# Performance work log

Hardware: AMD Instinct MI355X
Metric: run time of the kernel (lower is better)

The kernel has to match this reference:

```python
import jax, jax.numpy as jnp
import numpy as np

S, B, C, H, W = 16, 64, 128, 11, 11
P = H * W
N_ITER = 3
EPS = 1e-5


def setup_inputs() -> dict:
    key = jax.random.key(0)
    ks = jax.random.split(key, 12)
    w = lambda k, shape: jax.random.normal(k, shape, jnp.float32) * 0.02
    return {
        "x": jax.random.normal(ks[0], (S, B, C, H, W), jnp.float32),
        # intra-attention 1x1 convs (stored as [out,in] matrices)
        "wq": w(ks[1], (C, C)), "bq": jnp.zeros((C,), jnp.float32),
        "wk": w(ks[2], (C, C)), "bk": jnp.zeros((C,), jnp.float32),
        "wv": w(ks[3], (C, C)), "bv": jnp.zeros((C,), jnp.float32),
        "intra_alpha": jnp.float32(1.0),
        # inter-message path
        "w_msg": w(ks[4], (C, C + 1)), "b_msg": jnp.zeros((C,), jnp.float32),
        "w_lin": w(ks[5], (C, C)),
        "weight": jnp.float32(0.5),
        "w_gate": w(ks[6], (C, C)), "b_gate": jnp.zeros((C,), jnp.float32),
        # ConvGRU 3x3 convs
        "w_zr": w(ks[7], (2 * C, 2 * C, 3, 3)), "b_zr": jnp.zeros((2 * C,), jnp.float32),
        "w_h": w(ks[8], (C, 2 * C, 3, 3)), "b_h": jnp.zeros((C,), jnp.float32),
        # LayerNorm over [C,11,11]
        "ln_gamma": jnp.ones((C, H, W), jnp.float32),
        "ln_beta": jnp.zeros((C, H, W), jnp.float32),
    }


def reference(x, wq, bq, wk, bk, wv, bv, intra_alpha, w_msg, b_msg, w_lin,
              weight, w_gate, b_gate, w_zr, b_zr, w_h, b_h, ln_gamma, ln_beta):
    scale = C ** -0.5

    def c1(t, wgt, bias):  # 1x1 conv on [S,B,Cin,H,W] -> [S,B,Cout,H,W]
        return jnp.einsum('sbchw,oc->sbohw', t, wgt) + bias[:, None, None]

    def conv3(t, wgt, bias):  # 3x3 'SAME' conv on [N,Cin,H,W]
        y = jax.lax.conv_general_dilated(
            t, wgt, (1, 1), 'SAME', dimension_numbers=('NCHW', 'OIHW', 'NCHW'))
        return y + bias[None, :, None, None]

    # chain-graph neighbor validity masks (|i-j| == 1)
    mask_l = (jnp.arange(S) >= 1).astype(x.dtype)[:, None, None, None, None]
    mask_r = (jnp.arange(S) <= S - 2).astype(x.dtype)[:, None, None, None, None]

    h = x
    for _ in range(N_ITER):
        # ---- intra spatial self-attention (per node, over P=H*W tokens) ----
        q = c1(h, wq, bq).reshape(S, B, C, P)
        k = c1(h, wk, bk).reshape(S, B, C, P)
        v = c1(h, wv, bv).reshape(S, B, C, P)
        att = jax.nn.softmax(jnp.einsum('sbcp,sbcq->sbpq', q, k) * scale, axis=-1)
        intra = jnp.einsum('sbpq,sbcq->sbcp', att, v).reshape(S, B, C, H, W)
        intra = intra_alpha * intra + h

        # ---- inter gated message attention from chain neighbors ----
        xf = h.reshape(S, B, C, P)

        def gated_msg(y, edge_val):
            ef = jnp.full((S, B, 1, H, W), edge_val, h.dtype)  # edge feature i-j
            yy = c1(jnp.concatenate([y, ef], axis=2), w_msg, b_msg).reshape(S, B, C, P)
            yy = jnp.einsum('sbcp,dc->sbdp', yy, w_lin)  # Linear (no bias)
            a = jax.nn.softmax(jnp.einsum('sbcp,sbcq->sbpq', xf, yy), axis=-1)
            m = jnp.einsum('sbpq,sbcq->sbcp', a, yy).reshape(S, B, C, H, W)
            g = jax.nn.sigmoid(c1(m, w_gate, b_gate).mean(axis=(-2, -1), keepdims=True))
            return m * g

        y_left = jnp.concatenate([jnp.zeros_like(h[:1]), h[:-1]], axis=0)   # h[i-1], edge +1
        y_right = jnp.concatenate([h[1:], jnp.zeros_like(h[:1])], axis=0)   # h[i+1], edge -1
        inter = gated_msg(y_left, 1.0) * mask_l + gated_msg(y_right, -1.0) * mask_r

        comb = weight * intra + (1.0 - weight) * inter

        # ---- ConvGRU update (fold S into batch) ----
        xg = comb.reshape(S * B, C, H, W)
        hg = h.reshape(S * B, C, H, W)
        zr = jax.nn.sigmoid(conv3(jnp.concatenate([xg, hg], axis=1), w_zr, b_zr))
        z, r = zr[:, :C], zr[:, C:]
        h_hat = jnp.tanh(conv3(jnp.concatenate([xg, r * hg], axis=1), w_h, b_h))
        h_new = ((1 - z) * hg + z * h_hat).reshape(S, B, C, H, W)

        # ---- residual + LayerNorm over [C,H,W] ----
        nh = h_new + h
        mu = nh.mean(axis=(-3, -2, -1), keepdims=True)
        var = nh.var(axis=(-3, -2, -1), keepdims=True)
        h = (nh - mu) * jax.lax.rsqrt(var + EPS) * ln_gamma + ln_beta
    return h
```

## Files before the change

### kernel.cpp

```cpp
#include <hip/hip_runtime.h>
#include <hip/hip_bf16.h>

#define S_   16
#define B_   64
#define SBn  1024
#define C_   128
#define P_   121
#define CP_  15488
static const long NEl = 15859712L;

typedef __hip_bfloat16 bf16t;
typedef __attribute__((ext_vector_type(8))) short bf16x8;
typedef __attribute__((ext_vector_type(4))) float f32x4;
typedef __attribute__((ext_vector_type(4))) unsigned short us4;

__device__ __forceinline__ float ldb(const bf16t* p){ return __bfloat162float(*p); }
__device__ __forceinline__ float b2f(unsigned short u){ unsigned x=((unsigned)u)<<16; float f; __builtin_memcpy(&f,&x,4); return f; }
__device__ __forceinline__ unsigned short f2bu(float v){ __hip_bfloat16 b=__float2bfloat16(v); unsigned short u; __builtin_memcpy(&u,&b,2); return u; }
__device__ __forceinline__ float ldin(const void* s, long i, int f){
    return f ? ((const float*)s)[i] : b2f(((const unsigned short*)s)[i]);
}

__global__ void detect_kernel(const unsigned short* __restrict__ x, int* __restrict__ flag){
    if(blockIdx.x==0 && threadIdx.x==0){
        int crazy=0;
        for(int i=0;i<512;i++){
            unsigned e=(x[i]>>7)&0xFF;
            if(e!=0 && (e<64 || e>191)) crazy++;
        }
        *flag=(crazy>40)?1:0;
    }
}

__global__ void cvt_kernel(float* __restrict__ dst, const void* __restrict__ src, long n, const int* __restrict__ flag){
    long i=(long)blockIdx.x*blockDim.x+threadIdx.x;
    long st=(long)gridDim.x*blockDim.x;
    int f=*flag;
    for(;i<n;i+=st) dst[i]=ldin(src,i,f);
}

__global__ __launch_bounds__(256) void cvtT_kernel(bf16t* __restrict__ hT, const void* __restrict__ x, const int* __restrict__ flag){
    __shared__ bf16t tl[CP_];
    int sb=blockIdx.x, t=threadIdx.x; int f=*flag;
    for(int i=t;i<CP_;i+=256)
        tl[i]=__float2bfloat16(ldin(x,(long)sb*CP_+i,f));
    __syncthreads();
    bf16t* ho=hT+(size_t)sb*CP_;
    for(int j=t;j<CP_;j+=256){
        int p=j>>7, c=j&127;
        ho[j]=tl[c*P_+p];
    }
}

__global__ __launch_bounds__(128) void prep_msg_kernel(float* __restrict__ W2, float* __restrict__ b2l, float* __restrict__ b2r,
        const void* __restrict__ wlin, const void* __restrict__ wmsg, const void* __restrict__ bmsg, const int* __restrict__ flag){
    int d=blockIdx.x, c=threadIdx.x; int f=*flag;
    float acc=0.f;
    for(int o2=0;o2<C_;o2++) acc += ldin(wlin,(long)d*C_+o2,f)*ldin(wmsg,(long)o2*(C_+1)+c,f);
    W2[d*C_+c]=acc;
    if(c<2){
        float e=(c==0)?1.f:-1.f; float a=0.f;
        for(int o2=0;o2<C_;o2++) a += ldin(wlin,(long)d*C_+o2,f)*(ldin(bmsg,o2,f)+e*ldin(wmsg,(long)o2*(C_+1)+C_,f));
        if(c==0) b2l[d]=a; else b2r[d]=a;
    }
}

template<int RAW>
__global__ void prep_w1t(bf16t* __restrict__ dst, const void* __restrict__ src, const int* __restrict__ flag){
    int idx=blockIdx.x*blockDim.x+threadIdx.x;
    if(idx>=16384) return;
    int r=idx&31, oc=(idx>>5)&127, icb=idx>>12;
    float v = RAW? ldin(src,(long)oc*C_+icb*32+r,*flag) : ((const float*)src)[(long)oc*C_+icb*32+r];
    dst[idx]=__float2bfloat16(v);
}

__global__ void prep_w3t(bf16t* __restrict__ dst, const void* __restrict__ src, const int* __restrict__ flag, int OC){
    int idx=blockIdx.x*blockDim.x+threadIdx.x;
    int tot=OC*2304;
    if(idx>=tot) return;
    int r=idx&31; int rest=idx>>5; int oc=rest%OC; int g2=rest/OC; int icb=g2&7, tap=g2>>3;
    float v=ldin(src,((long)(oc*256+icb*32+r))*9+tap,*flag);
    dst[idx]=__float2bfloat16(v);
}

__global__ void prep_gbt(float* __restrict__ gamT, float* __restrict__ betT,
                         const void* __restrict__ gam, const void* __restrict__ bet, const int* __restrict__ flag){
    int idx=blockIdx.x*blockDim.x+threadIdx.x;
    if(idx>=CP_) return;
    int c=idx/P_, p=idx-c*P_; int f=*flag;
    gamT[p*C_+c]=ldin(gam,idx,f);
    betT[p*C_+c]=ldin(bet,idx,f);
}

__global__ void prep_wgt(float* __restrict__ wgT, float* __restrict__ bg2,
                         const void* __restrict__ wg, const void* __restrict__ bg, const int* __restrict__ flag){
    int idx=blockIdx.x*blockDim.x+threadIdx.x;
    int f=*flag;
    if(idx<16384){ int k=idx>>7, c=idx&127; wgT[idx]=ldin(wg,(long)c*C_+k,f); }
    if(idx<128) bg2[idx]=ldin(bg,idx,f);
}

__device__ __forceinline__ void gemm24r(f32x4 (&acc)[4][2],
    const bf16t* __restrict__ Wt, const bf16x8 (&hreg)[4][2],
    int ocr,int l15,int kg)
{
    #pragma unroll
    for(int i=0;i<4;i++){
        #pragma unroll
        for(int j=0;j<2;j++) acc[i][j]=(f32x4){0.f,0.f,0.f,0.f};
    }
    #pragma unroll
    for(int kc=0;kc<4;kc++){
        bf16x8 a[4];
        #pragma unroll
        for(int mt=0;mt<4;mt++) a[mt]=*(const bf16x8*)(Wt+((size_t)(kc*C_+ocr*64+mt*16+l15))*32+kg*8);
        #pragma unroll
        for(int mt=0;mt<4;mt++){
            #pragma unroll
            for(int nt=0;nt<2;nt++)
                acc[mt][nt]=__builtin_amdgcn_mfma_f32_16x16x32_bf16(a[mt],hreg[kc][nt],acc[mt][nt],0,0,0);
        }
    }
}

__device__ __forceinline__ void msg_phase(
    f32x4 (&res)[8], const bf16t* __restrict__ hT, int sb, int shift,
    const bf16t* __restrict__ W2T, const float* __restrict__ b2e,
    const float* __restrict__ wgT, const float* __restrict__ bgf, float w1m,
    const bf16x8 (&areg)[4],
    bf16t* LA, bf16t* LB, float* fl,
    int t,int w,int l15,int kg,int ocr,int pcr)
{
    __syncthreads();
    const bf16t* hsp=hT+(size_t)(sb+shift)*CP_;
    bf16x8 hregS[4][2];
    #pragma unroll
    for(int kc=0;kc<4;kc++){
        #pragma unroll
        for(int nt=0;nt<2;nt++)
            hregS[kc][nt]=*(const bf16x8*)(hsp+(size_t)(pcr*32+nt*16+l15)*C_+kc*32+kg*8);
    }
    f32x4 acc[4][2];
    gemm24r(acc,W2T,hregS,ocr,l15,kg);
    #pragma unroll
    for(int mt=0;mt<4;mt++){
        int oc0=ocr*64+mt*16+kg*4;
        #pragma unroll
        for(int nt=0;nt<2;nt++){
            int p=pcr*32+nt*16+l15;
            us4 pk;
            #pragma unroll
            for(int r=0;r<4;r++){
                float v=acc[mt][nt][r]+b2e[oc0+r];
                pk[r]=f2bu(v);
                LB[(oc0+r)*136+p]=__float2bfloat16(p<P_? v : 0.f);
            }
            *(us4*)(LA+p*136+oc0)=pk;
        }
    }
    __syncthreads();
    int m0=w*16;
    f32x4 s[8];
    #pragma unroll
    for(int nt=0;nt<8;nt++) s[nt]=(f32x4){0.f,0.f,0.f,0.f};
    #pragma unroll
    for(int kc=0;kc<4;kc++){
        #pragma unroll
        for(int nt=0;nt<8;nt++){
            bf16x8 b=*(const bf16x8*)(LA+(size_t)(nt*16+l15)*136+kc*32+kg*8);
            s[nt]=__builtin_amdgcn_mfma_f32_16x16x32_bf16(areg[kc],b,s[nt],0,0,0);
        }
    }
    if(l15>=9){
        #pragma unroll
        for(int r=0;r<4;r++) s[7][r]=-3.0e38f;
    }
    #pragma unroll
    for(int r=0;r<4;r++){
        float mx=s[0][r];
        #pragma unroll
        for(int nt=1;nt<8;nt++) mx=fmaxf(mx,s[nt][r]);
        #pragma unroll
        for(int o=1;o<16;o<<=1) mx=fmaxf(mx,__shfl_xor(mx,o));
        float sm=0.f;
        #pragma unroll
        for(int nt=0;nt<8;nt++){ float e=__expf(s[nt][r]-mx); s[nt][r]=e; sm+=e; }
        #pragma unroll
        for(int o=1;o<16;o<<=1) sm+=__shfl_xor(sm,o);
        float rs=1.f/sm;
        #pragma unroll
        for(int nt=0;nt<8;nt++) s[nt][r]*=rs;
    }
    __syncthreads();
    #pragma unroll
    for(int r=0;r<4;r++){
        int pr=m0+kg*4+r;
        #pragma unroll
        for(int nt=0;nt<8;nt++) LA[pr*136+nt*16+l15]=__float2bfloat16(s[nt][r]);
    }
    __syncthreads();
    f32x4 o[8];
    #pragma unroll
    for(int nt=0;nt<8;nt++) o[nt]=(f32x4){0.f,0.f,0.f,0.f};
    #pragma unroll
    for(int jc=0;jc<4;jc++){
        bf16x8 a=*(const bf16x8*)(LB+(size_t)(m0+l15)*136+jc*32+kg*8);
        #pragma unroll
        for(int nt=0;nt<8;nt++){
            bf16x8 b=*(const bf16x8*)(LA+(size_t)(nt*16+l15)*136+jc*32+kg*8);
            o[nt]=__builtin_amdgcn_mfma_f32_16x16x32_bf16(a,b,o[nt],0,0,0);
        }
    }
    int c0=m0+kg*4;
    #pragma unroll
    for(int r=0;r<4;r++){
        float sm=0.f;
        #pragma unroll
        for(int nt=0;nt<8;nt++){ float v=o[nt][r]; if(nt==7&&l15>8) v=0.f; sm+=v; }
        sm+=__shfl_xor(sm,1); sm+=__shfl_xor(sm,2); sm+=__shfl_xor(sm,4); sm+=__shfl_xor(sm,8);
        if(l15==0) fl[c0+r]=sm*(1.f/121.f);
    }
    __syncthreads();
    if(t<C_){
        float a=bgf[t];
        #pragma unroll 8
        for(int k=0;k<C_;k++) a+=wgT[k*C_+t]*fl[k];
        fl[C_+t]=1.f/(1.f+__expf(-a));
    }
    __syncthreads();
    float gg[4];
    #pragma unroll
    for(int r=0;r<4;r++) gg[r]=fl[C_+c0+r];
    #pragma unroll
    for(int nt=0;nt<8;nt++){
        #pragma unroll
        for(int r=0;r<4;r++) res[nt][r]+=w1m*o[nt][r]*gg[r];
    }
}

__global__ __launch_bounds__(512) void attn_all(
    bf16t* __restrict__ comb, const bf16t* __restrict__ hT,
    const bf16t* __restrict__ WqT, const bf16t* __restrict__ WkT, const bf16t* __restrict__ WvT,
    const float* __restrict__ bq, const float* __restrict__ bk, const float* __restrict__ bv,
    const bf16t* __restrict__ W2T, const float* __restrict__ b2l, const float* __restrict__ b2r,
    const float* __restrict__ wgT, const float* __restrict__ bgf,
    const float* __restrict__ alphap, const float* __restrict__ wp)
{
    __shared__ bf16t LA[128*136];
    __shared__ bf16t LB[128*136];
    __shared__ float fl[256];
    int sb=blockIdx.x, t=threadIdx.x, lane=t&63, w=t>>6;
    int l15=lane&15, kg=lane>>4;
    const bf16t* hp=hT+(size_t)sb*CP_;
    int ocr=w>>2, pcr=w&3;
    int m0=w*16;
    bf16x8 hreg[4][2];
    #pragma unroll
    for(int kc=0;kc<4;kc++){
        #pragma unroll
        for(int nt=0;nt<2;nt++)
            hreg[kc][nt]=*(const bf16x8*)(hp+(size_t)(pcr*32+nt*16+l15)*C_+kc*32+kg*8);
    }
    bf16x8 areg[4];
    #pragma unroll
    for(int kc=0;kc<4;kc++)
        areg[kc]=*(const bf16x8*)(hp+(size_t)(m0+l15)*C_+kc*32+kg*8);

    f32x4 acc[4][2];
    gemm24r(acc,WqT,hreg,ocr,l15,kg);
    #pragma unroll
    for(int mt=0;mt<4;mt++){
        int oc0=ocr*64+mt*16+kg*4;
        #pragma unroll
        for(int nt=0;nt<2;nt++){
            int p=pcr*32+nt*16+l15;
            us4 pk;
            #pragma unroll
            for(int r=0;r<4;r++) pk[r]=f2bu(acc[mt][nt][r]+bq[oc0+r]);
            *(us4*)(LA+p*136+oc0)=pk;
        }
    }
    gemm24r(acc,WkT,hreg,ocr,l15,kg);
    #pragma unroll
    for(int mt=0;mt<4;mt++){
        int oc0=ocr*64+mt*16+kg*4;
        #pragma unroll
        for(int nt=0;nt<2;nt++){
            int p=pcr*32+nt*16+l15;
            us4 pk;
            #pragma unroll
            for(int r=0;r<4;r++) pk[r]=f2bu(acc[mt][nt][r]+bk[oc0+r]);
            *(us4*)(LB+p*136+oc0)=pk;
        }
    }
    __syncthreads();
    f32x4 s[8];
    #pragma unroll
    for(int nt=0;nt<8;nt++) s[nt]=(f32x4){0.f,0.f,0.f,0.f};
    #pragma unroll
    for(int kc=0;kc<4;kc++){
        bf16x8 a=*(const bf16x8*)(LA+(size_t)(m0+l15)*136+kc*32+kg*8);
        #pragma unroll
        for(int nt=0;nt<8;nt++){
            bf16x8 b=*(const bf16x8*)(LB+(size_t)(nt*16+l15)*136+kc*32+kg*8);
            s[nt]=__builtin_amdgcn_mfma_f32_16x16x32_bf16(a,b,s[nt],0,0,0);
        }
    }
    const float scale=0.08838834764831845f;
    #pragma unroll
    for(int nt=0;nt<8;nt++){
        #pragma unroll
        for(int r=0;r<4;r++) s[nt][r]*=scale;
    }
    if(l15>=9){
        #pragma unroll
        for(int r=0;r<4;r++) s[7][r]=-3.0e38f;
    }
    #pragma unroll
    for(int r=0;r<4;r++){
        float mx=s[0][r];
        #pragma unroll
        for(int nt=1;nt<8;nt++) mx=fmaxf(mx,s[nt][r]);
        #pragma unroll
        for(int o=1;o<16;o<<=1) mx=fmaxf(mx,__shfl_xor(mx,o));
        float sm=0.f;
        #pragma unroll
        for(int nt=0;nt<8;nt++){ float e=__expf(s[nt][r]-mx); s[nt][r]=e; sm+=e; }
        #pragma unroll
        for(int o=1;o<16;o<<=1) sm+=__shfl_xor(sm,o);
        float rs=1.f/sm;
        #pragma unroll
        for(int nt=0;nt<8;nt++) s[nt][r]*=rs;
    }
    __syncthreads();
    gemm24r(acc,WvT,hreg,ocr,l15,kg);
    #pragma unroll
    for(int mt=0;mt<4;mt++){
        int oc0=ocr*64+mt*16+kg*4;
        #pragma unroll
        for(int nt=0;nt<2;nt++){
            int p=pcr*32+nt*16+l15;
            #pragma unroll
            for(int r=0;r<4;r++)
                LA[(oc0+r)*136+p]=__float2bfloat16(p<P_? acc[mt][nt][r]+bv[oc0+r] : 0.f);
        }
    }
    #pragma unroll
    for(int r=0;r<4;r++){
        int pr=m0+kg*4+r;
        #pragma unroll
        for(int nt=0;nt<8;nt++) LB[pr*136+nt*16+l15]=__float2bfloat16(s[nt][r]);
    }
    __syncthreads();
    f32x4 res[8];
    #pragma unroll
    for(int nt=0;nt<8;nt++) res[nt]=(f32x4){0.f,0.f,0.f,0.f};
    #pragma unroll
    for(int jc=0;jc<4;jc++){
        bf16x8 a=*(const bf16x8*)(LA+(size_t)(m0+l15)*136+jc*32+kg*8);
        #pragma unroll
        for(int nt=0;nt<8;nt++){
            bf16x8 b=*(const bf16x8*)(LB+(size_t)(nt*16+l15)*136+jc*32+kg*8);
            res[nt]=__builtin_amdgcn_mfma_f32_16x16x32_bf16(a,b,res[nt],0,0,0);
        }
    }
    float al=*alphap, wv=*wp, w1m=1.f-wv;
    int c0=m0+kg*4;
    #pragma unroll
    for(int nt=0;nt<8;nt++){
        int p=nt*16+l15;
        int pc=(p<P_)?p:(P_-1);
        us4 hv=*(const us4*)(hp+(size_t)pc*C_+c0);
        #pragma unroll
        for(int r=0;r<4;r++) res[nt][r]=wv*(al*res[nt][r]+b2f(hv[r]));
    }
    if(sb>=B_)
        msg_phase(res,hT,sb,-B_,W2T,b2l,wgT,bgf,w1m,areg,LA,LB,fl,t,w,l15,kg,ocr,pcr);
    if(sb<SBn-B_)
        msg_phase(res,hT,sb, B_,W2T,b2r,wgT,bgf,w1m,areg,LA,LB,fl,t,w,l15,kg,ocr,pcr);
    __syncthreads();
    unsigned short* tl=(unsigned short*)LA;
    #pragma unroll
    for(int nt=0;nt<8;nt++){
        int p=nt*16+l15;
        if(p>=P_) continue;
        us4 pk;
        #pragma unroll
        for(int r=0;r<4;r++) pk[r]=f2bu(res[nt][r]);
        *(us4*)(tl+p*C_+c0)=pk;
    }
    __syncthreads();
    bf16t* ob=comb+(size_t)sb*CP_;
    for(int j=t;j<1936;j+=512)
        *(bf16x8*)(ob+j*8)=*(const bf16x8*)(tl+j*8);
}

#define LOADA2(bidx, widx) { \
    _Pragma("unroll") \
    for(int mt=0;mt<2;mt++) abuf[bidx][mt]=*(const bf16x8*)(Wt+(size_t)(widx)*(OC*32)+mt*512+base_lane); }
#define STEP2(lbase, bidx, doff) { \
    bf16x8 bb[4]; \
    _Pragma("unroll") \
    for(int nt=0;nt<4;nt++) bb[nt]=*(const bf16x8*)((lbase)+boff[nt]+(doff)); \
    __builtin_amdgcn_s_setprio(1); \
    _Pragma("unroll") \
    for(int mt=0;mt<2;mt++){ \
        _Pragma("unroll") \
        for(int nt=0;nt<4;nt++) \
            acc[mt][nt]=__builtin_amdgcn_mfma_f32_16x16x32_bf16(abuf[bidx][mt],bb[nt],acc[mt][nt],0,0,0); } \
    __builtin_amdgcn_s_setprio(0); }

#define SLOADZ2(stg) { \
    const bf16t* s0=(((stg)<2)? in0T:in1T)+(size_t)sb0*CP_+((stg)&1)*64; \
    const bf16t* s1=s0+CP_; \
    sreg[0]=*(const bf16x8*)(s0+(size_t)spA*C_+(t&7)*8); \
    if(sv1) sreg[1]=*(const bf16x8*)(s0+(size_t)spB*C_+(t&7)*8); \
    sreg[2]=*(const bf16x8*)(s1+(size_t)spA*C_+(t&7)*8); \
    if(sv1) sreg[3]=*(const bf16x8*)(s1+(size_t)spB*C_+(t&7)*8); }
#define SWRITEZ2(lbase) { \
    *(bf16x8*)((lbase)+spixA*72+(t&7)*8)=sreg[0]; \
    if(sv1) *(bf16x8*)((lbase)+spixB*72+(t&7)*8)=sreg[1]; \
    *(bf16x8*)((lbase)+12176+spixA*72+(t&7)*8)=sreg[2]; \
    if(sv1) *(bf16x8*)((lbase)+12176+spixB*72+(t&7)*8)=sreg[3]; }
#define STEPZ2(lbase, bidx, doff) { \
    bf16x8 bb0[4], bb1[4]; \
    _Pragma("unroll") \
    for(int nt=0;nt<4;nt++){ \
        bb0[nt]=*(const bf16x8*)((lbase)+boff[nt]+(doff)); \
        bb1[nt]=*(const bf16x8*)((lbase)+12176+boff[nt]+(doff)); } \
    __builtin_amdgcn_s_setprio(1); \
    _Pragma("unroll") \
    for(int mt=0;mt<2;mt++){ \
        _Pragma("unroll") \
        for(int nt=0;nt<4;nt++){ \
            accA[mt][nt]=__builtin_amdgcn_mfma_f32_16x16x32_bf16(abuf[bidx][mt],bb0[nt],accA[mt][nt],0,0,0); \
            accB[mt][nt]=__builtin_amdgcn_mfma_f32_16x16x32_bf16(abuf[bidx][mt],bb1[nt],accB[mt][nt],0,0,0); } } \
    __builtin_amdgcn_s_setprio(0); }

__global__ __launch_bounds__(512) void conv3_zr2(
    bf16t* __restrict__ o0, bf16t* __restrict__ o1,
    const bf16t* __restrict__ in0T, const bf16t* __restrict__ in1T,
    const bf16t* __restrict__ Wt, const float* __restrict__ bias,
    const bf16t* __restrict__ hTb)
{
    constexpr int OC=256;
    __shared__ bf16t lin[4*12176];
    int sb0=(int)blockIdx.x*2, ocb=(int)blockIdx.y*128;
    int t=threadIdx.x, lane=t&63, w=t>>6;
    int ocr=w>>1, pcr=w&1, l15=lane&15, kg=lane>>4;
    int boff[4]; bool pv_[4];
    #pragma unroll
    for(int nt=0;nt<4;nt++){
        int p=pcr*64+nt*16+l15;
        pv_[nt]=(p<P_); int pc=pv_[nt]?p:(P_-1);
        boff[nt]=((pc/11)*13+(pc%11))*72+kg*8;
    }
    f32x4 accA[2][4], accB[2][4];
    #pragma unroll
    for(int i=0;i<2;i++){
        #pragma unroll
        for(int j=0;j<4;j++){ accA[i][j]=(f32x4){0.f,0.f,0.f,0.f}; accB[i][j]=(f32x4){0.f,0.f,0.f,0.f}; }
    }
    int base_lane=(ocb+ocr*32+l15)*32+kg*8;
    bf16x8 abuf[4][2];
    bf16x8 sreg[4];
    bool sv1=((t+512)<968);
    int spA=t>>3, spB=(t+512)>>3;
    if(spB>120) spB=120;
    int spixA=(spA/11+1)*13+(spA%11)+1;
    int spixB=(spB/11+1)*13+(spB%11)+1;
    LOADA2(0,0); LOADA2(1,1); LOADA2(2,8); LOADA2(3,9);
    SLOADZ2(0);
    {
        bf16x8 z;
        #pragma unroll
        for(int e=0;e<8;e++) z[e]=0;
        for(int i=t;i<1536;i+=512){
            int tile=i/384; int i2=i-tile*384;
            int bi=i2>>3, cc=(i2&7)*8;
            int pix;
            if(bi<13) pix=bi;
            else if(bi<26) pix=156+(bi-13);
            else { int j2=bi-26; pix=(1+(j2>>1))*13+((j2&1)?12:0); }
            *(bf16x8*)(lin+tile*12176+pix*72+cc)=z;
        }
    }
    SWRITEZ2(lin);
    __syncthreads();
    #pragma unroll
    for(int st=0; st<4; ++st){
        if(st<3) SLOADZ2(st+1);
        bf16t* lbase=lin+(st&1)*24352;
        #pragma unroll
        for(int k=0;k<18;k++){
            int s=st*18+k;
            int tap=k>>1, l=k&1;
            int doff=((tap/3)*13+(tap%3))*72+l*32;
            STEPZ2(lbase, s&3, doff);
            if(s<68){
                int s4=s+4, st4=s4/18, k4=s4-st4*18, tap4=k4>>1, l4=k4&1;
                LOADA2(s&3, tap4*8+st4*2+l4);
            }
        }
        if(st<3){ SWRITEZ2(lin+((st+1)&1)*24352); }
        __syncthreads();
    }
    unsigned short* tl=(unsigned short*)lin;
    bf16t* obase=(ocb==0? o0 : o1);
    const float* bs=bias+(ocb==0?0:128);
    #pragma unroll
    for(int mt=0;mt<2;mt++){
        int ocl=ocr*32+mt*16+kg*4;
        #pragma unroll
        for(int nt=0;nt<4;nt++){
            if(!pv_[nt]) continue;
            int p=pcr*64+nt*16+l15;
            us4 pk;
            if(ocb==0){
                #pragma unroll
                for(int r=0;r<4;r++){ float a=accA[mt][nt][r]+bs[ocl+r]; pk[r]=f2bu(1.f/(1.f+__expf(-a))); }
            }else{
                size_t tb=(size_t)sb0*CP_+(size_t)p*C_+ocl;
                us4 hv=*(const us4*)(hTb+tb);
                #pragma unroll
                for(int r=0;r<4;r++){ float a=accA[mt][nt][r]+bs[ocl+r]; float sg=1.f/(1.f+__expf(-a)); pk[r]=f2bu(sg*b2f(hv[r])); }
            }
            *(us4*)(tl+p*C_+ocl)=pk;
        }
    }
    __syncthreads();
    {
        bf16t* ob=obase+(size_t)sb0*CP_;
        for(int j=t;j<1936;j+=512)
            *(bf16x8*)(ob+j*8)=*(const bf16x8*)(tl+j*8);
    }
    __syncthreads();
    #pragma unroll
    for(int mt=0;mt<2;mt++){
        int ocl=ocr*32+mt*16+kg*4;
        #pragma unroll
        for(int nt=0;nt<4;nt++){
            if(!pv_[nt]) continue;
            int p=pcr*64+nt*16+l15;
            us4 pk;
            if(ocb==0){
                #pragma unroll
                for(int r=0;r<4;r++){ float a=accB[mt][nt][r]+bs[ocl+r]; pk[r]=f2bu(1.f/(1.f+__expf(-a))); }
            }else{
                size_t tb=(size_t)(sb0+1)*CP_+(size_t)p*C_+ocl;
                us4 hv=*(const us4*)(hTb+tb);
                #pragma unroll
                for(int r=0;r<4;r++){ float a=accB[mt][nt][r]+bs[ocl+r]; float sg=1.f/(1.f+__expf(-a)); pk[r]=f2bu(sg*b2f(hv[r])); }
            }
            *(us4*)(tl+p*C_+ocl)=pk;
        }
    }
    __syncthreads();
    {
        bf16t* ob=obase+(size_t)(sb0+1)*CP_;
        for(int j=t;j<1936;j+=512)
            *(bf16x8*)(ob+j*8)=*(const bf16x8*)(tl+j*8);
    }
}

#define SLOADH(stg) { \
    const bf16t* ssrc=(((stg)<2)? in0T:in1T)+(size_t)sb*CP_+((stg)&1)*64; \
    sreg[0]=*(const bf16x8*)(ssrc+(size_t)(t>>3)*C_+(t&7)*8); \
    if(sv1) sreg[1]=*(const bf16x8*)(ssrc+(size_t)sp1*C_+(t&7)*8); }
#define SWRITEH(lbase) { \
    *(bf16x8*)((lbase)+spix0*72+(t&7)*8)=sreg[0]; \
    if(sv1) *(bf16x8*)((lbase)+spix1*72+(t&7)*8)=sreg[1]; }

__global__ __launch_bounds__(512,4) void conv3_hh(
    bf16t* __restrict__ o0,
    const bf16t* __restrict__ in0T, const bf16t* __restrict__ in1T,
    const bf16t* __restrict__ Wt, const float* __restrict__ bias,
    const bf16t* __restrict__ zT, const bf16t* __restrict__ hTb,
    const float* __restrict__ gamT, const float* __restrict__ betT)
{
    constexpr int OC=128;
    __shared__ bf16t lin[2*12176];
    __shared__ float red[16];
    int sb=blockIdx.x;
    int t=threadIdx.x, lane=t&63, w=t>>6;
    int ocr=w>>1, pcr=w&1, l15=lane&15, kg=lane>>4;
    int boff[4]; bool pv_[4];
    #pragma unroll
    for(int nt=0;nt<4;nt++){
        int p=pcr*64+nt*16+l15;
        pv_[nt]=(p<P_); int pc=pv_[nt]?p:(P_-1);
        boff[nt]=((pc/11)*13+(pc%11))*72+kg*8;
    }
    f32x4 acc[2][4];
    #pragma unroll
    for(int i=0;i<2;i++){
        #pragma unroll
        for(int j=0;j<4;j++) acc[i][j]=(f32x4){0.f,0.f,0.f,0.f};
    }
    int base_lane=(ocr*32+l15)*32+kg*8;
    bf16x8 abuf[4][2];
    bf16x8 sreg[2];
    bool sv1=((t+512)<968);
    int sp0=t>>3, sp1=(t+512)>>3;
    if(sp1>120) sp1=120;
    int spix0=(sp0/11+1)*13+(sp0%11)+1;
    int spix1=(sp1/11+1)*13+(sp1%11)+1;
    LOADA2(0,0); LOADA2(1,1); LOADA2(2,8); LOADA2(3,9);
    SLOADH(0);
    {
        bf16x8 z;
        #pragma unroll
        for(int e=0;e<8;e++) z[e]=0;
        for(int i=t;i<768;i+=512){
            int half=i>=384; int i2=i-half*384;
            int bi=i2>>3, cc=(i2&7)*8;
            int pix;
            if(bi<13) pix=bi;
            else if(bi<26) pix=156+(bi-13);
            else { int j2=bi-26; pix=(1+(j2>>1))*13+((j2&1)?12:0); }
            *(bf16x8*)(lin+half*12176+pix*72+cc)=z;
        }
    }
    SWRITEH(lin);
    __syncthreads();
    #pragma unroll
    for(int st=0; st<4; ++st){
        if(st<3) SLOADH(st+1);
        bf16t* lbase=lin+(st&1)*12176;
        #pragma unroll
        for(int k=0;k<18;k++){
            int s=st*18+k;
            int tap=k>>1, l=k&1;
            int doff=((tap/3)*13+(tap%3))*72+l*32;
            STEP2(lbase, s&3, doff);
            if(s<68){
                int s4=s+4, st4=s4/18, k4=s4-st4*18, tap4=k4>>1, l4=k4&1;
                LOADA2(s&3, tap4*8+st4*2+l4);
            }
        }
        if(st<3){ SWRITEH(lin+((st+1)&1)*12176); }
        __syncthreads();
    }
    float ls=0.f, ls2=0.f;
    #pragma unroll
    for(int mt=0;mt<2;mt++){
        int ocl=ocr*32+mt*16+kg*4;
        #pragma unroll
        for(int nt=0;nt<4;nt++){
            if(!pv_[nt]) continue;
            int p=pcr*64+nt*16+l15;
            size_t tb=(size_t)sb*CP_+(size_t)p*C_+ocl;
            us4 hv=*(const us4*)(hTb+tb);
            us4 zv=*(const us4*)(zT+tb);
            us4 pk;
            #pragma unroll
            for(int r=0;r<4;r++){
                float a=acc[mt][nt][r]+bias[ocl+r];
                float ht=tanhf(a);
                float z=b2f(zv[r]), h=b2f(hv[r]);
                unsigned short u=f2bu((1.f-z)*h+z*ht+h);
                pk[r]=u;
                float nr=b2f(u); ls+=nr; ls2+=nr*nr;
            }
            *(us4*)((unsigned short*)lin + p*C_+ocl)=pk;
        }
    }
    #pragma unroll
    for(int o=32;o;o>>=1){ ls+=__shfl_xor(ls,o); ls2+=__shfl_xor(ls2,o); }
    if(lane==0){ red[w]=ls; red[8+w]=ls2; }
    __syncthreads();
    float Sx=0.f,Sx2=0.f;
    #pragma unroll
    for(int i=0;i<8;i++){ Sx+=red[i]; Sx2+=red[8+i]; }
    float mu=Sx*(1.f/(float)CP_);
    float var=Sx2*(1.f/(float)CP_)-mu*mu;
    float rstd=rsqrtf(var+1e-5f);
    bf16t* ho=o0+(size_t)sb*CP_;
    const unsigned short* tl=(const unsigned short*)lin;
    for(int j=t;j<1936;j+=512){
        int base=j*8;
        bf16x8 ovec;
        #pragma unroll
        for(int e=0;e<8;e++){
            float v=(b2f(tl[base+e])-mu)*rstd*gamT[base+e]+betT[base+e];
            ovec[e]=(short)f2bu(v);
        }
        *(bf16x8*)(ho+base)=ovec;
    }
}

__global__ __launch_bounds__(256) void finalT_kernel(void* __restrict__ fout, const bf16t* __restrict__ hT, const int* __restrict__ flag){
    __shared__ bf16t tl[CP_];
    int sb=blockIdx.x, t=threadIdx.x, f=*flag;
    for(int i=t;i<CP_;i+=256) tl[i]=hT[(size_t)sb*CP_+i];
    __syncthreads();
    for(int i=t;i<CP_;i+=256){
        int c=i/P_, p=i-c*P_;
        float v=ldb(tl+p*C_+c);
        size_t oi=(size_t)sb*CP_+i;
        if(f) ((float*)fout)[oi]=v;
        else  ((bf16t*)fout)[oi]=__float2bfloat16(v);
    }
}

extern "C" void kernel_launch(void* const* d_in, const int* in_sizes, int n_in,
                              void* d_out, int out_size, void* d_ws, size_t ws_size,
                              hipStream_t stream) {
    (void)in_sizes; (void)n_in; (void)out_size;
    char* base=(char*)d_ws;
    size_t off=0;
    auto alloc=[&](size_t bytes){ void* p=base+off; off+=(bytes+255)&~(size_t)255; return p; };
    bf16t* b1=(bf16t*)alloc((size_t)NEl*2+8192);
    bf16t* b2=(bf16t*)alloc((size_t)NEl*2+8192);
    bf16t* b3=(bf16t*)alloc((size_t)NEl*2+8192);
    bf16t* b4=(bf16t*)d_out;
    bf16t* wqT=(bf16t*)alloc(16384*2);
    bf16t* wkT=(bf16t*)alloc(16384*2);
    bf16t* wvT=(bf16t*)alloc(16384*2);
    bf16t* w2T=(bf16t*)alloc(16384*2);
    bf16t* wzrT=(bf16t*)alloc((size_t)589824*2);
    bf16t* whT =(bf16t*)alloc((size_t)294912*2);
    float* W2f=(float*)alloc(16384*4);
    float* b2l=(float*)alloc(128*4); float* b2r=(float*)alloc(128*4);
    float* bqf=(float*)alloc(128*4); float* bkf=(float*)alloc(128*4); float* bvf=(float*)alloc(128*4);
    float* bzrf=(float*)alloc(256*4); float* bhf=(float*)alloc(128*4);
    float* gamT=(float*)alloc(15488*4); float* betT=(float*)alloc(15488*4);
    float* wgTf=(float*)alloc(16384*4); float* bgf2=(float*)alloc(128*4);
    float* alphaf=(float*)alloc(4); float* weightf=(float*)alloc(4);
    int* flag=(int*)alloc(4);
    if(ws_size<off) return;

    detect_kernel<<<1,64,0,stream>>>((const unsigned short*)d_in[0],flag);
    cvtT_kernel<<<SBn,256,0,stream>>>(b1,d_in[0],flag);
    prep_w1t<1><<<64,256,0,stream>>>(wqT,d_in[1],flag);
    cvt_kernel<<<1,128,0,stream>>>(bqf,d_in[2],128,flag);
    prep_w1t<1><<<64,256,0,stream>>>(wkT,d_in[3],flag);
    cvt_kernel<<<1,128,0,stream>>>(bkf,d_in[4],128,flag);
    prep_w1t<1><<<64,256,0,stream>>>(wvT,d_in[5],flag);
    cvt_kernel<<<1,128,0,stream>>>(bvf,d_in[6],128,flag);
    cvt_kernel<<<1,64,0,stream>>>(alphaf,d_in[7],1,flag);
    prep_msg_kernel<<<C_,C_,0,stream>>>(W2f,b2l,b2r,d_in[10],d_in[8],d_in[9],flag);
    prep_w1t<0><<<64,256,0,stream>>>(w2T,W2f,flag);
    cvt_kernel<<<1,64,0,stream>>>(weightf,d_in[11],1,flag);
    prep_wgt<<<64,256,0,stream>>>(wgTf,bgf2,d_in[12],d_in[13],flag);
    prep_w3t<<<(256*2304+255)/256,256,0,stream>>>(wzrT,d_in[14],flag,256);
    cvt_kernel<<<1,256,0,stream>>>(bzrf,d_in[15],256,flag);
    prep_w3t<<<(128*2304+255)/256,256,0,stream>>>(whT,d_in[16],flag,128);
    cvt_kernel<<<1,128,0,stream>>>(bhf,d_in[17],128,flag);
    prep_gbt<<<(CP_+255)/256,256,0,stream>>>(gamT,betT,d_in[18],d_in[19],flag);

    for(int it=0; it<3; ++it){
        attn_all<<<SBn,512,0,stream>>>(b2,b1,wqT,wkT,wvT,bqf,bkf,bvf,
                                       w2T,b2l,b2r,wgTf,bgf2,alphaf,weightf);
        conv3_zr2<<<dim3(SBn/2,2),512,0,stream>>>(b4,b3,b2,b1,wzrT,bzrf,b1);
        conv3_hh<<<SBn,512,0,stream>>>(b1,b2,b3,whT,bhf,b4,b1,gamT,betT);
    }
    finalT_kernel<<<SBn,256,0,stream>>>(d_out,b1,flag);
}
```

Baseline: 1.341 ms.

## Process two graph nodes per attention block to interleave independent work

The attention kernel now handles two consecutive (s,b) nodes per 512-thread block, with doubled LDS buffers, and the grid is halved. The per-node GEMM, softmax and message phases are interleaved across the two nodes, so the block runs half as many barriers per node and has more independent MFMA work between them. The cost is double the LDS (about 140KB) and more registers, which lowers occupancy and may cause spills. The boundary checks sb0>=B_ and sb0<SBn-B_ stay correct because both nodes in a pair share the same s.

```diff
diff --git a/kernel.cpp b/kernel.cpp
--- a/kernel.cpp
+++ b/kernel.cpp
@@ -7,6 +7,7 @@
 #define C_   128
 #define P_   121
 #define CP_  15488
+#define LTS  17408
 static const long NEl = 15859712L;
 
 typedef __hip_bfloat16 bf16t;
@@ -123,122 +124,141 @@
     }
 }
 
-__device__ __forceinline__ void msg_phase(
-    f32x4 (&res)[8], const bf16t* __restrict__ hT, int sb, int shift,
+__device__ __forceinline__ void msg_phase2(
+    f32x4 (&res)[2][8], const bf16t* __restrict__ hT, int sb0, int shift,
     const bf16t* __restrict__ W2T, const float* __restrict__ b2e,
     const float* __restrict__ wgT, const float* __restrict__ bgf, float w1m,
-    const bf16x8 (&areg)[4],
-    bf16t* LA, bf16t* LB, float* fl,
+    const bf16x8 (&areg)[2][4],
+    bf16t (*LA)[LTS], bf16t (*LB)[LTS], float (*fl)[256],
     int t,int w,int l15,int kg,int ocr,int pcr)
 {
     __syncthreads();
-    const bf16t* hsp=hT+(size_t)(sb+shift)*CP_;
-    bf16x8 hregS[4][2];
-    #pragma unroll
-    for(int kc=0;kc<4;kc++){
-        #pragma unroll
-        for(int nt=0;nt<2;nt++)
-            hregS[kc][nt]=*(const bf16x8*)(hsp+(size_t)(pcr*32+nt*16+l15)*C_+kc*32+kg*8);
-    }
-    f32x4 acc[4][2];
-    gemm24r(acc,W2T,hregS,ocr,l15,kg);
-    #pragma unroll
-    for(int mt=0;mt<4;mt++){
-        int oc0=ocr*64+mt*16+kg*4;
-        #pragma unroll
-        for(int nt=0;nt<2;nt++){
-            int p=pcr*32+nt*16+l15;
-            us4 pk;
-            #pragma unroll
-            for(int r=0;r<4;r++){
-                float v=acc[mt][nt][r]+b2e[oc0+r];
-                pk[r]=f2bu(v);
-                LB[(oc0+r)*136+p]=__float2bfloat16(p<P_? v : 0.f);
-            }
-            *(us4*)(LA+p*136+oc0)=pk;
-        }
-    }
-    __syncthreads();
     int m0=w*16;
-    f32x4 s[8];
-    #pragma unroll
-    for(int nt=0;nt<8;nt++) s[nt]=(f32x4){0.f,0.f,0.f,0.f};
-    #pragma unroll
-    for(int kc=0;kc<4;kc++){
+    #pragma unroll
+    for(int io=0;io<2;io++){
+        const bf16t* hsp=hT+(size_t)(sb0+io+shift)*CP_;
+        bf16x8 hregS[4][2];
+        #pragma unroll
+        for(int kc=0;kc<4;kc++){
+            #pragma unroll
+            for(int nt=0;nt<2;nt++)
+                hregS[kc][nt]=*(const bf16x8*)(hsp+(size_t)(pcr*32+nt*16+l15)*C_+kc*32+kg*8);
+        }
+        f32x4 acc[4][2];
+        gemm24r(acc,W2T,hregS,ocr,l15,kg);
+        #pragma unroll
+        for(int mt=0;mt<4;mt++){
+            int oc0=ocr*64+mt*16+kg*4;
+            #pragma unroll
+            for(int nt=0;nt<2;nt++){
+                int p=pcr*32+nt*16+l15;
+                us4 pk;
+                #pragma unroll
+                for(int r=0;r<4;r++){
+                    float v=acc[mt][nt][r]+b2e[oc0+r];
+                    pk[r]=f2bu(v);
+                    LB[io][(oc0+r)*136+p]=__float2bfloat16(p<P_? v : 0.f);
+                }
+                *(us4*)(LA[io]+p*136+oc0)=pk;
+            }
+        }
+    }
+    __syncthreads();
+    f32x4 s[2][8];
+    #pragma unroll
+    for(int io=0;io<2;io++){
+        #pragma unroll
+        for(int nt=0;nt<8;nt++) s[io][nt]=(f32x4){0.f,0.f,0.f,0.f};
+        #pragma unroll
+        for(int kc=0;kc<4;kc++){
+            #pragma unroll
+            for(int nt=0;nt<8;nt++){
+                bf16x8 b=*(const bf16x8*)(LA[io]+(size_t)(nt*16+l15)*136+kc*32+kg*8);
+                s[io][nt]=__builtin_amdgcn_mfma_f32_16x16x32_bf16(areg[io][kc],b,s[io][nt],0,0,0);
+            }
+        }
+        if(l15>=9){
+            #pragma unroll
+            for(int r=0;r<4;r++) s[io][7][r]=-3.0e38f;
+        }
+        #pragma unroll
+        for(int r=0;r<4;r++){
+            float mx=s[io][0][r];
+            #pragma unroll
+            for(int nt=1;nt<8;nt++) mx=fmaxf(mx,s[io][nt][r]);
+            #pragma unroll
+            for(int o=1;o<16;o<<=1) mx=fmaxf(mx,__shfl_xor(mx,o));
+            float sm=0.f;
+            #pragma unroll
+            for(int nt=0;nt<8;nt++){ float e=__expf(s[io][nt][r]-mx); s[io][nt][r]=e; sm+=e; }
+            #pragma unroll
+            for(int o=1;o<16;o<<=1) sm+=__shfl_xor(sm,o);
+            float rs=1.f/sm;
+            #pragma unroll
+            for(int nt=0;nt<8;nt++) s[io][nt][r]*=rs;
+        }
+    }
+    __syncthreads();
+    #pragma unroll
+    for(int io=0;io<2;io++){
+        #pragma unroll
+        for(int r=0;r<4;r++){
+            int pr=m0+kg*4+r;
+            #pragma unroll
+            for(int nt=0;nt<8;nt++) LA[io][pr*136+nt*16+l15]=__float2bfloat16(s[io][nt][r]);
+        }
+    }
+    __syncthreads();
+    f32x4 o[2][8];
+    #pragma unroll
+    for(int io=0;io<2;io++){
+        #pragma unroll
+        for(int nt=0;nt<8;nt++) o[io][nt]=(f32x4){0.f,0.f,0.f,0.f};
+        #pragma unroll
+        for(int jc=0;jc<4;jc++){
+            bf16x8 a=*(const bf16x8*)(LB[io]+(size_t)(m0+l15)*136+jc*32+kg*8);
+            #pragma unroll
+            for(int nt=0;nt<8;nt++){
+                bf16x8 b=*(const bf16x8*)(LA[io]+(size_t)(nt*16+l15)*136+jc*32+kg*8);
+                o[io][nt]=__builtin_amdgcn_mfma_f32_16x16x32_bf16(a,b,o[io][nt],0,0,0);
+            }
+        }
+    }
+    int c0=m0+kg*4;
+    #pragma unroll
+    for(int io=0;io<2;io++){
+        #pragma unroll
+        for(int r=0;r<4;r++){
+            float sm=0.f;
+            #pragma unroll
+            for(int nt=0;nt<8;nt++){ float v=o[io][nt][r]; if(nt==7&&l15>8) v=0.f; sm+=v; }
+            sm+=__shfl_xor(sm,1); sm+=__shfl_xor(sm,2); sm+=__shfl_xor(sm,4); sm+=__shfl_xor(sm,8);
+            if(l15==0) fl[io][c0+r]=sm*(1.f/121.f);
+        }
+    }
+    __syncthreads();
+    if(t<256){
+        int which=t>>7, c=t&127;
+        float a=bgf[c];
+        #pragma unroll 8
+        for(int k=0;k<C_;k++) a+=wgT[k*C_+c]*fl[which][k];
+        fl[which][C_+c]=1.f/(1.f+__expf(-a));
+    }
+    __syncthreads();
+    #pragma unroll
+    for(int io=0;io<2;io++){
+        float gg[4];
+        #pragma unroll
+        for(int r=0;r<4;r++) gg[r]=fl[io][C_+c0+r];
         #pragma unroll
         for(int nt=0;nt<8;nt++){
-            bf16x8 b=*(const bf16x8*)(LA+(size_t)(nt*16+l15)*136+kc*32+kg*8);
-            s[nt]=__builtin_amdgcn_mfma_f32_16x16x32_bf16(areg[kc],b,s[nt],0,0,0);
-        }
-    }
-    if(l15>=9){
-        #pragma unroll
-        for(int r=0;r<4;r++) s[7][r]=-3.0e38f;
-    }
-    #pragma unroll
-    for(int r=0;r<4;r++){
-        float mx=s[0][r];
-        #pragma unroll
-        for(int nt=1;nt<8;nt++) mx=fmaxf(mx,s[nt][r]);
-        #pragma unroll
-        for(int o=1;o<16;o<<=1) mx=fmaxf(mx,__shfl_xor(mx,o));
-        float sm=0.f;
-        #pragma unroll
-        for(int nt=0;nt<8;nt++){ float e=__expf(s[nt][r]-mx); s[nt][r]=e; sm+=e; }
-        #pragma unroll
-        for(int o=1;o<16;o<<=1) sm+=__shfl_xor(sm,o);
-        float rs=1.f/sm;
-        #pragma unroll
-        for(int nt=0;nt<8;nt++) s[nt][r]*=rs;
-    }
-    __syncthreads();
-    #pragma unroll
-    for(int r=0;r<4;r++){
-        int pr=m0+kg*4+r;
-        #pragma unroll
-        for(int nt=0;nt<8;nt++) LA[pr*136+nt*16+l15]=__float2bfloat16(s[nt][r]);
-    }
-    __syncthreads();
-    f32x4 o[8];
-    #pragma unroll
-    for(int nt=0;nt<8;nt++) o[nt]=(f32x4){0.f,0.f,0.f,0.f};
-    #pragma unroll
-    for(int jc=0;jc<4;jc++){
-        bf16x8 a=*(const bf16x8*)(LB+(size_t)(m0+l15)*136+jc*32+kg*8);
-        #pragma unroll
-        for(int nt=0;nt<8;nt++){
-            bf16x8 b=*(const bf16x8*)(LA+(size_t)(nt*16+l15)*136+jc*32+kg*8);
-            o[nt]=__builtin_amdgcn_mfma_f32_16x16x32_bf16(a,b,o[nt],0,0,0);
-        }
-    }
-    int c0=m0+kg*4;
-    #pragma unroll
-    for(int r=0;r<4;r++){
-        float sm=0.f;
-        #pragma unroll
-        for(int nt=0;nt<8;nt++){ float v=o[nt][r]; if(nt==7&&l15>8) v=0.f; sm+=v; }
-        sm+=__shfl_xor(sm,1); sm+=__shfl_xor(sm,2); sm+=__shfl_xor(sm,4); sm+=__shfl_xor(sm,8);
-        if(l15==0) fl[c0+r]=sm*(1.f/121.f);
-    }
-    __syncthreads();
-    if(t<C_){
-        float a=bgf[t];
-        #pragma unroll 8
-        for(int k=0;k<C_;k++) a+=wgT[k*C_+t]*fl[k];
-        fl[C_+t]=1.f/(1.f+__expf(-a));
-    }
-    __syncthreads();
-    float gg[4];
-    #pragma unroll
-    for(int r=0;r<4;r++) gg[r]=fl[C_+c0+r];
-    #pragma unroll
-    for(int nt=0;nt<8;nt++){
-        #pragma unroll
-        for(int r=0;r<4;r++) res[nt][r]+=w1m*o[nt][r]*gg[r];
-    }
-}
-
-__global__ __launch_bounds__(512) void attn_all(
+            #pragma unroll
+            for(int r=0;r<4;r++) res[io][nt][r]+=w1m*o[io][nt][r]*gg[r];
+        }
+    }
+}
+
+__global__ __launch_bounds__(512) void attn2(
     bf16t* __restrict__ comb, const bf16t* __restrict__ hT,
     const bf16t* __restrict__ WqT, const bf16t* __restrict__ WkT, const bf16t* __restrict__ WvT,
     const float* __restrict__ bq, const float* __restrict__ bk, const float* __restrict__ bv,
@@ -246,153 +266,178 @@
     const float* __restrict__ wgT, const float* __restrict__ bgf,
     const float* __restrict__ alphap, const float* __restrict__ wp)
 {
-    __shared__ bf16t LA[128*136];
-    __shared__ bf16t LB[128*136];
-    __shared__ float fl[256];
-    int sb=blockIdx.x, t=threadIdx.x, lane=t&63, w=t>>6;
+    __shared__ bf16t LA[2][LTS];
+    __shared__ bf16t LB[2][LTS];
+    __shared__ float fl[2][256];
+    int sb0=(int)blockIdx.x*2, t=threadIdx.x, lane=t&63, w=t>>6;
     int l15=lane&15, kg=lane>>4;
-    const bf16t* hp=hT+(size_t)sb*CP_;
     int ocr=w>>2, pcr=w&3;
     int m0=w*16;
-    bf16x8 hreg[4][2];
+    const bf16t* hp0=hT+(size_t)sb0*CP_;
+    const bf16t* hp1=hp0+CP_;
+    bf16x8 hreg[2][4][2];
+    bf16x8 areg[2][4];
     #pragma unroll
     for(int kc=0;kc<4;kc++){
         #pragma unroll
-        for(int nt=0;nt<2;nt++)
-            hreg[kc][nt]=*(const bf16x8*)(hp+(size_t)(pcr*32+nt*16+l15)*C_+kc*32+kg*8);
-    }
-    bf16x8 areg[4];
-    #pragma unroll
-    for(int kc=0;kc<4;kc++)
-        areg[kc]=*(const bf16x8*)(hp+(size_t)(m0+l15)*C_+kc*32+kg*8);
-
-    f32x4 acc[4][2];
-    gemm24r(acc,WqT,hreg,ocr,l15,kg);
-    #pragma unroll
-    for(int mt=0;mt<4;mt++){
-        int oc0=ocr*64+mt*16+kg*4;
-        #pragma unroll
         for(int nt=0;nt<2;nt++){
-            int p=pcr*32+nt*16+l15;
-            us4 pk;
-            #pragma unroll
-            for(int r=0;r<4;r++) pk[r]=f2bu(acc[mt][nt][r]+bq[oc0+r]);
-            *(us4*)(LA+p*136+oc0)=pk;
-        }
-    }
-    gemm24r(acc,WkT,hreg,ocr,l15,kg);
-    #pragma unroll
-    for(int mt=0;mt<4;mt++){
-        int oc0=ocr*64+mt*16+kg*4;
-        #pragma unroll
-        for(int nt=0;nt<2;nt++){
-            int p=pcr*32+nt*16+l15;
-            us4 pk;
-            #pragma unroll
-            for(int r=0;r<4;r++) pk[r]=f2bu(acc[mt][nt][r]+bk[oc0+r]);
-            *(us4*)(LB+p*136+oc0)=pk;
-        }
-    }
-    __syncthreads();
-    f32x4 s[8];
-    #pragma unroll
-    for(int nt=0;nt<8;nt++) s[nt]=(f32x4){0.f,0.f,0.f,0.f};
-    #pragma unroll
-    for(int kc=0;kc<4;kc++){
-        bf16x8 a=*(const bf16x8*)(LA+(size_t)(m0+l15)*136+kc*32+kg*8);
+            hreg[0][kc][nt]=*(const bf16x8*)(hp0+(size_t)(pcr*32+nt*16+l15)*C_+kc*32+kg*8);
+            hreg[1][kc][nt]=*(const bf16x8*)(hp1+(size_t)(pcr*32+nt*16+l15)*C_+kc*32+kg*8);
+        }
+        areg[0][kc]=*(const bf16x8*)(hp0+(size_t)(m0+l15)*C_+kc*32+kg*8);
+        areg[1][kc]=*(const bf16x8*)(hp1+(size_t)(m0+l15)*C_+kc*32+kg*8);
+    }
+    #pragma unroll
+    for(int io=0;io<2;io++){
+        f32x4 acc[4][2];
+        gemm24r(acc,WqT,hreg[io],ocr,l15,kg);
+        #pragma unroll
+        for(int mt=0;mt<4;mt++){
+            int oc0=ocr*64+mt*16+kg*4;
+            #pragma unroll
+            for(int nt=0;nt<2;nt++){
+                int p=pcr*32+nt*16+l15;
+                us4 pk;
+                #pragma unroll
+                for(int r=0;r<4;r++) pk[r]=f2bu(acc[mt][nt][r]+bq[oc0+r]);
+                *(us4*)(LA[io]+p*136+oc0)=pk;
+            }
+        }
+        gemm24r(acc,WkT,hreg[io],ocr,l15,kg);
+        #pragma unroll
+        for(int mt=0;mt<4;mt++){
+            int oc0=ocr*64+mt*16+kg*4;
+            #pragma unroll
+            for(int nt=0;nt<2;nt++){
+                int p=pcr*32+nt*16+l15;
+                us4 pk;
+                #pragma unroll
+                for(int r=0;r<4;r++) pk[r]=f2bu(acc[mt][nt][r]+bk[oc0+r]);
+                *(us4*)(LB[io]+p*136+oc0)=pk;
+            }
+        }
+    }
+    __syncthreads();
+    const float scale=0.08838834764831845f;
+    f32x4 s[2][8];
+    #pragma unroll
+    for(int io=0;io<2;io++){
+        #pragma unroll
+        for(int nt=0;nt<8;nt++) s[io][nt]=(f32x4){0.f,0.f,0.f,0.f};
+        #pragma unroll
+        for(int kc=0;kc<4;kc++){
+            bf16x8 a=*(const bf16x8*)(LA[io]+(size_t)(m0+l15)*136+kc*32+kg*8);
+            #pragma unroll
+            for(int nt=0;nt<8;nt++){
+                bf16x8 b=*(const bf16x8*)(LB[io]+(size_t)(nt*16+l15)*136+kc*32+kg*8);
+                s[io][nt]=__builtin_amdgcn_mfma_f32_16x16x32_bf16(a,b,s[io][nt],0,0,0);
+            }
+        }
         #pragma unroll
         for(int nt=0;nt<8;nt++){
-            bf16x8 b=*(const bf16x8*)(LB+(size_t)(nt*16+l15)*136+kc*32+kg*8);
-            s[nt]=__builtin_amdgcn_mfma_f32_16x16x32_bf16(a,b,s[nt],0,0,0);
-        }
-    }
-    const float scale=0.08838834764831845f;
-    #pragma unroll
-    for(int nt=0;nt<8;nt++){
-        #pragma unroll
-        for(int r=0;r<4;r++) s[nt][r]*=scale;
-    }
-    if(l15>=9){
-        #pragma unroll
-        for(int r=0;r<4;r++) s[7][r]=-3.0e38f;
-    }
-    #pragma unroll
-    for(int r=0;r<4;r++){
-        float mx=s[0][r];
-        #pragma unroll
-        for(int nt=1;nt<8;nt++) mx=fmaxf(mx,s[nt][r]);
-        #pragma unroll
-        for(int o=1;o<16;o<<=1) mx=fmaxf(mx,__shfl_xor(mx,o));
-        float sm=0.f;
-        #pragma unroll
-        for(int nt=0;nt<8;nt++){ float e=__expf(s[nt][r]-mx); s[nt][r]=e; sm+=e; }
-        #pragma unroll
-        for(int o=1;o<16;o<<=1) sm+=__shfl_xor(sm,o);
-        float rs=1.f/sm;
-        #pragma unroll
-        for(int nt=0;nt<8;nt++) s[nt][r]*=rs;
-    }
-    __syncthreads();
-    gemm24r(acc,WvT,hreg,ocr,l15,kg);
-    #pragma unroll
-    for(int mt=0;mt<4;mt++){
-        int oc0=ocr*64+mt*16+kg*4;
-        #pragma unroll
-        for(int nt=0;nt<2;nt++){
-            int p=pcr*32+nt*16+l15;
-            #pragma unroll
-            for(int r=0;r<4;r++)
-                LA[(oc0+r)*136+p]=__float2bfloat16(p<P_? acc[mt][nt][r]+bv[oc0+r] : 0.f);
-        }
-    }
-    #pragma unroll
-    for(int r=0;r<4;r++){
-        int pr=m0+kg*4+r;
-        #pragma unroll
-        for(int nt=0;nt<8;nt++) LB[pr*136+nt*16+l15]=__float2bfloat16(s[nt][r]);
-    }
-    __syncthreads();
-    f32x4 res[8];
-    #pragma unroll
-    for(int nt=0;nt<8;nt++) res[nt]=(f32x4){0.f,0.f,0.f,0.f};
-    #pragma unroll
-    for(int jc=0;jc<4;jc++){
-        bf16x8 a=*(const bf16x8*)(LA+(size_t)(m0+l15)*136+jc*32+kg*8);
-        #pragma unroll
-        for(int nt=0;nt<8;nt++){
-            bf16x8 b=*(const bf16x8*)(LB+(size_t)(nt*16+l15)*136+jc*32+kg*8);
-            res[nt]=__builtin_amdgcn_mfma_f32_16x16x32_bf16(a,b,res[nt],0,0,0);
-        }
-    }
+            #pragma unroll
+            for(int r=0;r<4;r++) s[io][nt][r]*=scale;
+        }
+        if(l15>=9){
+            #pragma unroll
+            for(int r=0;r<4;r++) s[io][7][r]=-3.0e38f;
+        }
+        #pragma unroll
+        for(int r=0;r<4;r++){
+            float mx=s[io][0][r];
+            #pragma unroll
+            for(int nt=1;nt<8;nt++) mx=fmaxf(mx,s[io][nt][r]);
+            #pragma unroll
+            for(int o=1;o<16;o<<=1) mx=fmaxf(mx,__shfl_xor(mx,o));
+            float sm=0.f;
+            #pragma unroll
+            for(int nt=0;nt<8;nt++){ float e=__expf(s[io][nt][r]-mx); s[io][nt][r]=e; sm+=e; }
+            #pragma unroll
+            for(int o=1;o<16;o<<=1) sm+=__shfl_xor(sm,o);
+            float rs=1.f/sm;
+            #pragma unroll
+            for(int nt=0;nt<8;nt++) s[io][nt][r]*=rs;
+        }
+    }
+    __syncthreads();
+    #pragma unroll
+    for(int io=0;io<2;io++){
+        f32x4 acc[4][2];
+        gemm24r(acc,WvT,hreg[io],ocr,l15,kg);
+        #pragma unroll
+        for(int mt=0;mt<4;mt++){
+            int oc0=ocr*64+mt*16+kg*4;
+            #pragma unroll
+            for(int nt=0;nt<2;nt++){
+                int p=pcr*32+nt*16+l15;
+                #pragma unroll
+                for(int r=0;r<4;r++)
+                    LA[io][(oc0+r)*136+p]=__float2bfloat16(p<P_? acc[mt][nt][r]+bv[oc0+r] : 0.f);
+            }
+        }
+        #pragma unroll
+        for(int r=0;r<4;r++){
+            int pr=m0+kg*4+r;
+            #pragma unroll
+            for(int nt=0;nt<8;nt++) LB[io][pr*136+nt*16+l15]=__float2bfloat16(s[io][nt][r]);
+        }
+    }
+    __syncthreads();
     float al=*alphap, wv=*wp, w1m=1.f-wv;
     int c0=m0+kg*4;
-    #pragma unroll
-    for(int nt=0;nt<8;nt++){
-        int p=nt*16+l15;
-        int pc=(p<P_)?p:(P_-1);
-        us4 hv=*(const us4*)(hp+(size_t)pc*C_+c0);
-        #pragma unroll
-        for(int r=0;r<4;r++) res[nt][r]=wv*(al*res[nt][r]+b2f(hv[r]));
-    }
-    if(sb>=B_)
-        msg_phase(res,hT,sb,-B_,W2T,b2l,wgT,bgf,w1m,areg,LA,LB,fl,t,w,l15,kg,ocr,pcr);
-    if(sb<SBn-B_)
-        msg_phase(res,hT,sb, B_,W2T,b2r,wgT,bgf,w1m,areg,LA,LB,fl,t,w,l15,kg,ocr,pcr);
-    __syncthreads();
-    unsigned short* tl=(unsigned short*)LA;
-    #pragma unroll
-    for(int nt=0;nt<8;nt++){
-        int p=nt*16+l15;
-        if(p>=P_) continue;
-        us4 pk;
-        #pragma unroll
-        for(int r=0;r<4;r++) pk[r]=f2bu(res[nt][r]);
-        *(us4*)(tl+p*C_+c0)=pk;
-    }
-    __syncthreads();
-    bf16t* ob=comb+(size_t)sb*CP_;
-    for(int j=t;j<1936;j+=512)
-        *(bf16x8*)(ob+j*8)=*(const bf16x8*)(tl+j*8);
+    f32x4 res[2][8];
+    #pragma unroll
+    for(int io=0;io<2;io++){
+        #pragma unroll
+        for(int nt=0;nt<8;nt++) res[io][nt]=(f32x4){0.f,0.f,0.f,0.f};
+        #pragma unroll
+        for(int jc=0;jc<4;jc++){
+            bf16x8 a=*(const bf16x8*)(LA[io]+(size_t)(m0+l15)*136+jc*32+kg*8);
+            #pragma unroll
+            for(int nt=0;nt<8;nt++){
+                bf16x8 b=*(const bf16x8*)(LB[io]+(size_t)(nt*16+l15)*136+jc*32+kg*8);
+                res[io][nt]=__builtin_amdgcn_mfma_f32_16x16x32_bf16(a,b,res[io][nt],0,0,0);
+            }
+        }
+        const bf16t* hp=(io==0)?hp0:hp1;
+        #pragma unroll
+        for(int nt=0;nt<8;nt++){
+            int p=nt*16+l15;
+            int pc=(p<P_)?p:(P_-1);
+            us4 hv=*(const us4*)(hp+(size_t)pc*C_+c0);
+            #pragma unroll
+            for(int r=0;r<4;r++) res[io][nt][r]=wv*(al*res[io][nt][r]+b2f(hv[r]));
+        }
+    }
+    if(sb0>=B_)
+        msg_phase2(res,hT,sb0,-B_,W2T,b2l,wgT,bgf,w1m,areg,LA,LB,fl,t,w,l15,kg,ocr,pcr);
+    if(sb0<SBn-B_)
+        msg_phase2(res,hT,sb0, B_,W2T,b2r,wgT,bgf,w1m,areg,LA,LB,fl,t,w,l15,kg,ocr,pcr);
+    __syncthreads();
+    #pragma unroll
+    for(int io=0;io<2;io++){
+        unsigned short* tl=(unsigned short*)LA[io];
+        #pragma unroll
+        for(int nt=0;nt<8;nt++){
+            int p=nt*16+l15;
+            if(p>=P_) continue;
+            us4 pk;
+            #pragma unroll
+            for(int r=0;r<4;r++) pk[r]=f2bu(res[io][nt][r]);
+            *(us4*)(tl+p*C_+c0)=pk;
+        }
+    }
+    __syncthreads();
+    {
+        bf16t* ob0=comb+(size_t)sb0*CP_;
+        const unsigned short* t0=(const unsigned short*)LA[0];
+        for(int j=t;j<1936;j+=512)
+            *(bf16x8*)(ob0+j*8)=*(const bf16x8*)(t0+j*8);
+        bf16t* ob1=comb+(size_t)(sb0+1)*CP_;
+        const unsigned short* t1=(const unsigned short*)LA[1];
+        for(int j=t;j<1936;j+=512)
+            *(bf16x8*)(ob1+j*8)=*(const bf16x8*)(t1+j*8);
+    }
 }
 
 #define LOADA2(bidx, widx) { \
@@ -750,8 +795,8 @@
     prep_gbt<<<(CP_+255)/256,256,0,stream>>>(gamT,betT,d_in[18],d_in[19],flag);
 
     for(int it=0; it<3; ++it){
-        attn_all<<<SBn,512,0,stream>>>(b2,b1,wqT,wkT,wvT,bqf,bkf,bvf,
-                                       w2T,b2l,b2r,wgTf,bgf2,alphaf,weightf);
+        attn2<<<SBn/2,512,0,stream>>>(b2,b1,wqT,wkT,wvT,bqf,bkf,bvf,
+                                      w2T,b2l,b2r,wgTf,bgf2,alphaf,weightf);
         conv3_zr2<<<dim3(SBn/2,2),512,0,stream>>>(b4,b3,b2,b1,wzrT,bzrf,b1);
         conv3_hh<<<SBn,512,0,stream>>>(b1,b2,b3,whT,bhf,b4,b1,gamT,betT);
     }
```

New measurement: 1.300 ms. 3.0% less time.
